# Kernel tuning notes

Hardware: AMD Instinct MI355X
Metric: run time of the kernel (lower is better)

The kernel has to match this reference:

```python
import jax, jax.numpy as jnp
import numpy as np

EPS = 1e-5

def _bn(x, g, b, m, v):
    # inference-mode BatchNorm2d over NCHW
    inv = g / jnp.sqrt(v + EPS)
    return x * inv[None, :, None, None] + (b - m * inv)[None, :, None, None]

def _adder2d(x, w, stride, pad):
    # AdderNet 'convolution': out = -sum_{c,kh,kw} |patch - w|
    B, C, H, W = x.shape
    O, _, k, _ = w.shape
    xp = jnp.pad(x, ((0, 0), (0, 0), (pad, pad), (pad, pad)))
    Ho = (H + 2 * pad - k) // stride + 1
    Wo = (W + 2 * pad - k) // stride + 1
    # unfold: [B, C, k*k, Ho, Wo] with (C, kh, kw) ordering matching w.reshape
    cols = jnp.stack([xp[:, :, i:i + stride * Ho:stride, j:j + stride * Wo:stride]
                      for i in range(k) for j in range(k)], axis=2)
    cols = cols.reshape(B, C * k * k, Ho * Wo)            # [B, CKK, L]
    wf = w.reshape(O, C * k * k)                          # [O, CKK]
    out = -jnp.sum(jnp.abs(cols[:, None, :, :] - wf[None, :, :, None]), axis=2)  # [B,O,L]
    return out.reshape(B, O, Ho, Wo)

def setup_inputs() -> dict:
    key = jax.random.key(0)
    ks = jax.random.split(key, 16)
    C = 64
    return {
        "x": jax.random.normal(ks[0], (4, C, 32, 32), jnp.float32),
        "bn1_g": jax.random.uniform(ks[1], (C,), jnp.float32),
        "bn1_b": jax.random.normal(ks[2], (C,), jnp.float32),
        "bn1_m": jax.random.normal(ks[3], (C,), jnp.float32),
        "bn1_v": jax.random.uniform(ks[4], (C,), jnp.float32),
        "w1": jax.random.normal(ks[5], (C, C, 3, 3), jnp.float32),
        "bn2_g": jax.random.uniform(ks[6], (C,), jnp.float32),
        "bn2_b": jax.random.normal(ks[7], (C,), jnp.float32),
        "bn2_m": jax.random.normal(ks[8], (C,), jnp.float32),
        "bn2_v": jax.random.uniform(ks[9], (C,), jnp.float32),
        "w2": jax.random.normal(ks[10], (C, C, 3, 3), jnp.float32),
        "fc1_w": jax.random.normal(ks[11], (C // 16, C), jnp.float32) * 0.1,
        "fc1_b": jax.random.normal(ks[12], (C // 16,), jnp.float32) * 0.1,
        "fc2_w": jax.random.normal(ks[13], (C, C // 16), jnp.float32) * 0.1,
        "fc2_b": jax.random.normal(ks[14], (C,), jnp.float32) * 0.1,
    }

def reference(x, bn1_g, bn1_b, bn1_m, bn1_v, w1,
              bn2_g, bn2_b, bn2_m, bn2_v, w2,
              fc1_w, fc1_b, fc2_w, fc2_b):
    out = jax.nn.relu(_bn(x, bn1_g, bn1_b, bn1_m, bn1_v))
    shortcut = x  # stride==1 and in_planes==planes -> identity shortcut
    out = _adder2d(out, w1, 1, 1)
    out = _adder2d(jax.nn.relu(_bn(out, bn2_g, bn2_b, bn2_m, bn2_v)), w2, 1, 1)
    # SE gate: global avg pool -> fc1 -> relu -> fc2 -> sigmoid
    s = out.mean(axis=(2, 3))                              # [B, planes]
    h = jax.nn.relu(s @ fc1_w.T + fc1_b)
    g = jax.nn.sigmoid(h @ fc2_w.T + fc2_b)
    return out * g[:, :, None, None] + shortcut
```

## Files before the change

kernel.cpp:

```cpp
#include <hip/hip_runtime.h>
#include <math.h>

#define NELEM   262144
#define NPAIRW  18432
#define PIMG    1296
#define PPADN   165888
#define NPAIR   147968
#define EPS_BN  1e-5f
#define QSC     128.0f
#define QBIAS_F 16384.5f
#define QZ_W    0x40004000u
#define QINV    (1.0f / 128.0f)

__device__ __forceinline__ unsigned sad16(unsigned a, unsigned b, unsigned acc) {
    asm("v_sad_u16 %0, %1, %2, %0" : "+v"(acc) : "v"(a), "v"(b));
    return acc;
}

__device__ __forceinline__ unsigned qu(float v) {
    return (unsigned)(int)fmaf(v, QSC, QBIAS_F);
}

__global__ __launch_bounds__(256) void prep_kernel(
    const float* __restrict__ x,
    const float* __restrict__ g1, const float* __restrict__ b1,
    const float* __restrict__ m1, const float* __restrict__ v1,
    const float* __restrict__ w1,
    const float* __restrict__ g2, const float* __restrict__ b2,
    const float* __restrict__ m2, const float* __restrict__ v2,
    const float* __restrict__ w2,
    unsigned* __restrict__ qxp, unsigned* __restrict__ qout1p,
    unsigned* __restrict__ qw1p, unsigned* __restrict__ qw2p,
    float* __restrict__ bn2c, float* __restrict__ sbuf)
{
    int i = blockIdx.x * 256 + threadIdx.x;
    if (i < NPAIR) {
        int bp  = i / 1156;
        int rc  = i - bp * 1156;
        int r   = rc / 34;
        int col = rc - r * 34;
        bool interior = (r > 0 && r < 33 && col > 0 && col < 33);
        unsigned q = QZ_W;
        if (interior) {
            int b  = bp >> 5;
            int c0 = (bp & 31) * 2;
            float inv0 = g1[c0] * rsqrtf(v1[c0] + EPS_BN);
            float bet0 = b1[c0] - m1[c0] * inv0;
            float inv1 = g1[c0 + 1] * rsqrtf(v1[c0 + 1] + EPS_BN);
            float bet1 = b1[c0 + 1] - m1[c0 + 1] * inv1;
            int off = (b * 64 + c0) * 1024 + (r - 1) * 32 + (col - 1);
            float a0 = fmaxf(fmaf(x[off],        inv0, bet0), 0.f);
            float a1 = fmaxf(fmaf(x[off + 1024], inv1, bet1), 0.f);
            q = qu(a0) | (qu(a1) << 16);
        }
        int pidx = bp * PIMG + r * 36 + col;
        qxp[pidx] = q;
        if (!interior) qout1p[pidx] = QZ_W;
        return;
    }
    int k = i - NPAIR;
    if (k < NPAIRW) {
        int o   = k / 288;
        int rem = k - o * 288;
        int pr  = rem / 9;
        int kk  = rem - pr * 9;
        int woff = (o * 64 + pr * 2) * 9 + kk;
        qw1p[k] = qu(w1[woff]) | (qu(w1[woff + 9]) << 16);
        return;
    }
    int l = k - NPAIRW;
    if (l < NPAIRW) {
        int o   = l / 288;
        int rem = l - o * 288;
        int pr  = rem / 9;
        int kk  = rem - pr * 9;
        int woff = (o * 64 + pr * 2) * 9 + kk;
        qw2p[l] = qu(w2[woff]) | (qu(w2[woff + 9]) << 16);
        return;
    }
    int m = l - NPAIRW;
    if (m < 64) {
        float inv = g2[m] * rsqrtf(v2[m] + EPS_BN);
        bn2c[m]      = -inv * QINV;
        bn2c[m + 64] = b2[m] - m2[m] * inv;
        return;
    }
    int s = m - 64;
    if (s >= 0 && s < 256) sbuf[s] = 0.f;
}

template<int MODE>
__global__ __launch_bounds__(256, 4) void adder_kernel(
    const unsigned* __restrict__ qsrc, const unsigned* __restrict__ qwp,
    const float* __restrict__ bn2c,
    unsigned* __restrict__ qout, float* __restrict__ fout,
    float* __restrict__ sbuf)
{
    __shared__ unsigned wlds[2][32][12];
    __shared__ unsigned red[16][16][16];

    const int blk = blockIdx.x;
    const int sp  = blk & 7;
    const int og  = (blk >> 3) & 31;
    const int b   = blk >> 8;
    const int t   = threadIdx.x;
    const int pos = t & 15;
    const int cq  = t >> 4;
    const int y_i = pos >> 2;
    const int x0  = (pos & 3) * 8;

    const unsigned* base = qsrc + (size_t)(b * 32 + cq * 2) * PIMG
                                + (sp * 4 + y_i) * 36 + x0;

    unsigned p[2][3][12];
#pragma unroll
    for (int r = 0; r < 3; ++r) {
        uint4 a0 = *reinterpret_cast<const uint4*>(base + r * 36);
        uint4 a1 = *reinterpret_cast<const uint4*>(base + r * 36 + 4);
        uint4 a2 = *reinterpret_cast<const uint4*>(base + r * 36 + 8);
        p[0][r][0] = a0.x; p[0][r][1]  = a0.y; p[0][r][2]  = a0.z; p[0][r][3]  = a0.w;
        p[0][r][4] = a1.x; p[0][r][5]  = a1.y; p[0][r][6]  = a1.z; p[0][r][7]  = a1.w;
        p[0][r][8] = a2.x; p[0][r][9]  = a2.y; p[0][r][10] = a2.z; p[0][r][11] = a2.w;
    }

    for (int i = t; i < 576; i += 256) {
        int o_i = i / 288;
        int rem = i - o_i * 288;
        int pr  = rem / 9;
        int kk  = rem - pr * 9;
        wlds[o_i][pr][kk] = qwp[((og * 2 + o_i) * 32 + pr) * 9 + kk];
    }
    __syncthreads();

    unsigned acc[2][8];
#pragma unroll
    for (int oo = 0; oo < 2; ++oo)
#pragma unroll
        for (int xi = 0; xi < 8; ++xi) acc[oo][xi] = 0u;

#pragma unroll
    for (int j = 0; j < 2; ++j) {
        if (j == 0) {
            const unsigned* pn = base + PIMG;
#pragma unroll
            for (int r = 0; r < 3; ++r) {
                uint4 a0 = *reinterpret_cast<const uint4*>(pn + r * 36);
                uint4 a1 = *reinterpret_cast<const uint4*>(pn + r * 36 + 4);
                uint4 a2 = *reinterpret_cast<const uint4*>(pn + r * 36 + 8);
                p[1][r][0] = a0.x; p[1][r][1]  = a0.y; p[1][r][2]  = a0.z; p[1][r][3]  = a0.w;
                p[1][r][4] = a1.x; p[1][r][5]  = a1.y; p[1][r][6]  = a1.z; p[1][r][7]  = a1.w;
                p[1][r][8] = a2.x; p[1][r][9]  = a2.y; p[1][r][10] = a2.z; p[1][r][11] = a2.w;
            }
        }
        const int pr = cq * 2 + j;
#pragma unroll
        for (int oo = 0; oo < 2; ++oo) {
            uint4 wa = *reinterpret_cast<const uint4*>(&wlds[oo][pr][0]);
            uint4 wb = *reinterpret_cast<const uint4*>(&wlds[oo][pr][4]);
            unsigned w8 = wlds[oo][pr][8];
            unsigned wv[9] = {wa.x, wa.y, wa.z, wa.w,
                              wb.x, wb.y, wb.z, wb.w, w8};
#pragma unroll
            for (int kh = 0; kh < 3; ++kh)
#pragma unroll
                for (int kw = 0; kw < 3; ++kw) {
                    unsigned ww = wv[kh * 3 + kw];
#pragma unroll
                    for (int xi = 0; xi < 8; ++xi)
                        acc[oo][xi] = sad16(p[j][kh][xi + kw], ww, acc[oo][xi]);
                }
        }
    }

    {
        unsigned* dst = &red[cq][pos][0];
        *reinterpret_cast<uint4*>(dst + 0)  = make_uint4(acc[0][0], acc[0][1], acc[0][2], acc[0][3]);
        *reinterpret_cast<uint4*>(dst + 4)  = make_uint4(acc[0][4], acc[0][5], acc[0][6], acc[0][7]);
        *reinterpret_cast<uint4*>(dst + 8)  = make_uint4(acc[1][0], acc[1][1], acc[1][2], acc[1][3]);
        *reinterpret_cast<uint4*>(dst + 12) = make_uint4(acc[1][4], acc[1][5], acc[1][6], acc[1][7]);
    }
    __syncthreads();

    const int oo2 = t >> 7;
    const int s   = t & 127;
    const int yy2 = s >> 5;
    const int xx2 = s & 31;
    const int pp  = yy2 * 4 + (xx2 >> 3);
    const int z   = (oo2 << 3) | (xx2 & 7);
    unsigned total = 0;
#pragma unroll
    for (int q = 0; q < 16; ++q) total += red[q][pp][z];

    const int o    = og * 2 + oo2;
    const int gy   = sp * 4 + yy2;
    const float accf = (float)total;

    if (MODE == 0) {
        float a2 = fmaxf(fmaf(accf, bn2c[o], bn2c[o + 64]), 0.f);
        unsigned short qv = (unsigned short)(int)fmaf(a2, QSC, QBIAS_F);
        size_t widx = (size_t)(b * 32 + (o >> 1)) * PIMG + (gy + 1) * 36 + (xx2 + 1);
        reinterpret_cast<unsigned short*>(qout)[widx * 2 + (o & 1)] = qv;
    } else {
        float v = -accf * QINV;
        fout[((b * 64 + o) * 32 + gy) * 32 + xx2] = v;
        float sum = v;
#pragma unroll
        for (int off = 32; off > 0; off >>= 1)
            sum += __shfl_down(sum, off, 64);
        if ((t & 63) == 0) atomicAdd(&sbuf[b * 64 + o], sum);
    }
}

__global__ __launch_bounds__(256) void gate_kernel(
    const float* __restrict__ out2, const float* __restrict__ x,
    const float* __restrict__ sbuf,
    const float* __restrict__ fc1w, const float* __restrict__ fc1b,
    const float* __restrict__ fc2w, const float* __restrict__ fc2b,
    float* __restrict__ out)
{
    const int bo = blockIdx.x;
    const int b  = bo >> 6;
    const int o  = bo & 63;
    const int t  = threadIdx.x;

    __shared__ float ss[64];
    if (t < 64) ss[t] = sbuf[b * 64 + t] * (1.f / 1024.f);
    __syncthreads();

    float h[4];
#pragma unroll
    for (int j = 0; j < 4; ++j) {
        float a = fc1b[j];
#pragma unroll
        for (int c = 0; c < 64; ++c) a += ss[c] * fc1w[j * 64 + c];
        h[j] = fmaxf(a, 0.f);
    }
    float zz = fc2b[o];
#pragma unroll
    for (int j = 0; j < 4; ++j) zz += h[j] * fc2w[o * 4 + j];
    float g = 1.f / (1.f + __expf(-zz));

    const int base = bo * 1024 + t * 4;
    float4 v  = *reinterpret_cast<const float4*>(out2 + base);
    float4 xv = *reinterpret_cast<const float4*>(x + base);
    float4 r;
    r.x = v.x * g + xv.x;
    r.y = v.y * g + xv.y;
    r.z = v.z * g + xv.z;
    r.w = v.w * g + xv.w;
    *reinterpret_cast<float4*>(out + base) = r;
}

extern "C" void kernel_launch(void* const* d_in, const int* in_sizes, int n_in,
                              void* d_out, int out_size, void* d_ws, size_t ws_size,
                              hipStream_t stream)
{
    const float* x    = (const float*)d_in[0];
    const float* bn1g = (const float*)d_in[1];
    const float* bn1b = (const float*)d_in[2];
    const float* bn1m = (const float*)d_in[3];
    const float* bn1v = (const float*)d_in[4];
    const float* w1   = (const float*)d_in[5];
    const float* bn2g = (const float*)d_in[6];
    const float* bn2b = (const float*)d_in[7];
    const float* bn2m = (const float*)d_in[8];
    const float* bn2v = (const float*)d_in[9];
    const float* w2   = (const float*)d_in[10];
    const float* fc1w = (const float*)d_in[11];
    const float* fc1b = (const float*)d_in[12];
    const float* fc2w = (const float*)d_in[13];
    const float* fc2b = (const float*)d_in[14];

    unsigned* ws     = (unsigned*)d_ws;
    unsigned* qxp    = ws;
    unsigned* qout1p = ws + PPADN;
    float*    out2   = (float*)(ws + 2 * PPADN);
    unsigned* qw1p   = ws + 2 * PPADN + NELEM;
    unsigned* qw2p   = ws + 2 * PPADN + NELEM + NPAIRW;
    float*    bn2c   = (float*)(ws + 2 * PPADN + NELEM + 2 * NPAIRW);
    float*    sbuf   = (float*)(ws + 2 * PPADN + NELEM + 2 * NPAIRW + 128);

    prep_kernel<<<724, 256, 0, stream>>>(x, bn1g, bn1b, bn1m, bn1v, w1,
                                         bn2g, bn2b, bn2m, bn2v, w2,
                                         qxp, qout1p, qw1p, qw2p, bn2c, sbuf);
    adder_kernel<0><<<1024, 256, 0, stream>>>(qxp,    qw1p, bn2c, qout1p, nullptr, nullptr);
    adder_kernel<1><<<1024, 256, 0, stream>>>(qout1p, qw2p, nullptr, nullptr, out2, sbuf);
    gate_kernel<<<256, 256, 0, stream>>>(out2, x, sbuf, fc1w, fc1b, fc2w, fc2b,
                                         (float*)d_out);
}
```

Measured before the change: 109.6 us.

## Fuse prep into adder kernels, computing BN1 and quantization into an LDS tile

Removes the separate prep kernel. The first adder kernel now applies BN1, ReLU and quantization to x directly into a padded shared-memory tile, shared through a union with the reduction buffer. Each kernel quantizes its own weights on the fly, and the first also writes the halo border and zeroes the SE sum buffer. This drops one launch and the global round-trip of the quantized input, at the cost of redundant BN and weight quantization across blocks and a larger shared-memory footprint.

```diff
diff --git a/kernel.cpp b/kernel.cpp
--- a/kernel.cpp
+++ b/kernel.cpp
@@ -2,10 +2,8 @@
 #include <math.h>
 
 #define NELEM   262144
-#define NPAIRW  18432
 #define PIMG    1296
 #define PPADN   165888
-#define NPAIR   147968
 #define EPS_BN  1e-5f
 #define QSC     128.0f
 #define QBIAS_F 16384.5f
@@ -16,88 +14,25 @@
     asm("v_sad_u16 %0, %1, %2, %0" : "+v"(acc) : "v"(a), "v"(b));
     return acc;
 }
-
 __device__ __forceinline__ unsigned qu(float v) {
     return (unsigned)(int)fmaf(v, QSC, QBIAS_F);
 }
 
-__global__ __launch_bounds__(256) void prep_kernel(
+__global__ __launch_bounds__(256, 4) void adder1_kernel(
     const float* __restrict__ x,
     const float* __restrict__ g1, const float* __restrict__ b1,
     const float* __restrict__ m1, const float* __restrict__ v1,
     const float* __restrict__ w1,
     const float* __restrict__ g2, const float* __restrict__ b2,
     const float* __restrict__ m2, const float* __restrict__ v2,
-    const float* __restrict__ w2,
-    unsigned* __restrict__ qxp, unsigned* __restrict__ qout1p,
-    unsigned* __restrict__ qw1p, unsigned* __restrict__ qw2p,
-    float* __restrict__ bn2c, float* __restrict__ sbuf)
+    unsigned* __restrict__ qout, float* __restrict__ sbuf)
 {
-    int i = blockIdx.x * 256 + threadIdx.x;
-    if (i < NPAIR) {
-        int bp  = i / 1156;
-        int rc  = i - bp * 1156;
-        int r   = rc / 34;
-        int col = rc - r * 34;
-        bool interior = (r > 0 && r < 33 && col > 0 && col < 33);
-        unsigned q = QZ_W;
-        if (interior) {
-            int b  = bp >> 5;
-            int c0 = (bp & 31) * 2;
-            float inv0 = g1[c0] * rsqrtf(v1[c0] + EPS_BN);
-            float bet0 = b1[c0] - m1[c0] * inv0;
-            float inv1 = g1[c0 + 1] * rsqrtf(v1[c0 + 1] + EPS_BN);
-            float bet1 = b1[c0 + 1] - m1[c0 + 1] * inv1;
-            int off = (b * 64 + c0) * 1024 + (r - 1) * 32 + (col - 1);
-            float a0 = fmaxf(fmaf(x[off],        inv0, bet0), 0.f);
-            float a1 = fmaxf(fmaf(x[off + 1024], inv1, bet1), 0.f);
-            q = qu(a0) | (qu(a1) << 16);
-        }
-        int pidx = bp * PIMG + r * 36 + col;
-        qxp[pidx] = q;
-        if (!interior) qout1p[pidx] = QZ_W;
-        return;
-    }
-    int k = i - NPAIR;
-    if (k < NPAIRW) {
-        int o   = k / 288;
-        int rem = k - o * 288;
-        int pr  = rem / 9;
-        int kk  = rem - pr * 9;
-        int woff = (o * 64 + pr * 2) * 9 + kk;
-        qw1p[k] = qu(w1[woff]) | (qu(w1[woff + 9]) << 16);
-        return;
-    }
-    int l = k - NPAIRW;
-    if (l < NPAIRW) {
-        int o   = l / 288;
-        int rem = l - o * 288;
-        int pr  = rem / 9;
-        int kk  = rem - pr * 9;
-        int woff = (o * 64 + pr * 2) * 9 + kk;
-        qw2p[l] = qu(w2[woff]) | (qu(w2[woff + 9]) << 16);
-        return;
-    }
-    int m = l - NPAIRW;
-    if (m < 64) {
-        float inv = g2[m] * rsqrtf(v2[m] + EPS_BN);
-        bn2c[m]      = -inv * QINV;
-        bn2c[m + 64] = b2[m] - m2[m] * inv;
-        return;
-    }
-    int s = m - 64;
-    if (s >= 0 && s < 256) sbuf[s] = 0.f;
-}
-
-template<int MODE>
-__global__ __launch_bounds__(256, 4) void adder_kernel(
-    const unsigned* __restrict__ qsrc, const unsigned* __restrict__ qwp,
-    const float* __restrict__ bn2c,
-    unsigned* __restrict__ qout, float* __restrict__ fout,
-    float* __restrict__ sbuf)
-{
+    __shared__ union {
+        unsigned tile[32][6][36];
+        unsigned red[16][16][16];
+    } sh;
     __shared__ unsigned wlds[2][32][12];
-    __shared__ unsigned red[16][16][16];
+    __shared__ float binv[64], bbeta[64];
 
     const int blk = blockIdx.x;
     const int sp  = blk & 7;
@@ -109,6 +44,149 @@
     const int y_i = pos >> 2;
     const int x0  = (pos & 3) * 8;
 
+    if (t < 64) {
+        float inv = g1[t] * rsqrtf(v1[t] + EPS_BN);
+        binv[t]  = inv;
+        bbeta[t] = b1[t] - m1[t] * inv;
+    }
+    for (int i = t; i < 576; i += 256) {
+        int o_i = i / 288;
+        int rem = i - o_i * 288;
+        int pr  = rem / 9;
+        int kk  = rem - pr * 9;
+        int woff = ((og * 2 + o_i) * 64 + pr * 2) * 9 + kk;
+        wlds[o_i][pr][kk] = qu(w1[woff]) | (qu(w1[woff + 9]) << 16);
+    }
+    if (og == 0) {
+        for (int i = sp * 256 + t; i < 32 * 132; i += 2048) {
+            int pair = i / 132;
+            int rem  = i - pair * 132;
+            int row, col;
+            if (rem < 34)       { row = 0;            col = rem;       }
+            else if (rem < 68)  { row = 33;           col = rem - 34;  }
+            else if (rem < 100) { row = rem - 68 + 1; col = 0;         }
+            else                { row = rem - 100 + 1; col = 33;       }
+            qout[(size_t)(b * 32 + pair) * PIMG + row * 36 + col] = QZ_W;
+        }
+    }
+    if (blk == 0) sbuf[t] = 0.f;
+    __syncthreads();
+
+    for (int i = t; i < 192; i += 256) {
+        int pair = i / 6;
+        int row  = i - pair * 6;
+        int gy   = sp * 4 - 1 + row;
+        unsigned* dst = &sh.tile[pair][row][0];
+        if (gy < 0 || gy > 31) {
+            for (int col = 0; col < 34; ++col) dst[col] = QZ_W;
+        } else {
+            dst[0] = QZ_W; dst[33] = QZ_W;
+            const int c0 = pair * 2;
+            const float inv0 = binv[c0],     bet0 = bbeta[c0];
+            const float inv1 = binv[c0 + 1], bet1 = bbeta[c0 + 1];
+            const float* px = x + (size_t)((b * 64 + c0) * 32 + gy) * 32;
+#pragma unroll
+            for (int gx = 0; gx < 32; gx += 4) {
+                float4 u0 = *reinterpret_cast<const float4*>(px + gx);
+                float4 u1 = *reinterpret_cast<const float4*>(px + 1024 + gx);
+                dst[1 + gx]     = qu(fmaxf(fmaf(u0.x, inv0, bet0), 0.f))
+                                | (qu(fmaxf(fmaf(u1.x, inv1, bet1), 0.f)) << 16);
+                dst[1 + gx + 1] = qu(fmaxf(fmaf(u0.y, inv0, bet0), 0.f))
+                                | (qu(fmaxf(fmaf(u1.y, inv1, bet1), 0.f)) << 16);
+                dst[1 + gx + 2] = qu(fmaxf(fmaf(u0.z, inv0, bet0), 0.f))
+                                | (qu(fmaxf(fmaf(u1.z, inv1, bet1), 0.f)) << 16);
+                dst[1 + gx + 3] = qu(fmaxf(fmaf(u0.w, inv0, bet0), 0.f))
+                                | (qu(fmaxf(fmaf(u1.w, inv1, bet1), 0.f)) << 16);
+            }
+        }
+    }
+    __syncthreads();
+
+    unsigned acc[2][8];
+#pragma unroll
+    for (int oo = 0; oo < 2; ++oo)
+#pragma unroll
+        for (int xi = 0; xi < 8; ++xi) acc[oo][xi] = 0u;
+
+#pragma unroll
+    for (int j = 0; j < 2; ++j) {
+        const int pr = cq * 2 + j;
+        unsigned p[3][12];
+#pragma unroll
+        for (int r = 0; r < 3; ++r) {
+            uint4 a0 = *reinterpret_cast<const uint4*>(&sh.tile[pr][y_i + r][x0]);
+            uint4 a1 = *reinterpret_cast<const uint4*>(&sh.tile[pr][y_i + r][x0 + 4]);
+            uint4 a2 = *reinterpret_cast<const uint4*>(&sh.tile[pr][y_i + r][x0 + 8]);
+            p[r][0] = a0.x; p[r][1]  = a0.y; p[r][2]  = a0.z; p[r][3]  = a0.w;
+            p[r][4] = a1.x; p[r][5]  = a1.y; p[r][6]  = a1.z; p[r][7]  = a1.w;
+            p[r][8] = a2.x; p[r][9]  = a2.y; p[r][10] = a2.z; p[r][11] = a2.w;
+        }
+#pragma unroll
+        for (int oo = 0; oo < 2; ++oo) {
+            uint4 wa = *reinterpret_cast<const uint4*>(&wlds[oo][pr][0]);
+            uint4 wb = *reinterpret_cast<const uint4*>(&wlds[oo][pr][4]);
+            unsigned w8 = wlds[oo][pr][8];
+            unsigned wv[9] = {wa.x, wa.y, wa.z, wa.w,
+                              wb.x, wb.y, wb.z, wb.w, w8};
+#pragma unroll
+            for (int kh = 0; kh < 3; ++kh)
+#pragma unroll
+                for (int kw = 0; kw < 3; ++kw) {
+                    unsigned ww = wv[kh * 3 + kw];
+#pragma unroll
+                    for (int xi = 0; xi < 8; ++xi)
+                        acc[oo][xi] = sad16(p[kh][xi + kw], ww, acc[oo][xi]);
+                }
+        }
+    }
+
+    __syncthreads();
+    {
+        unsigned* dst = &sh.red[cq][pos][0];
+        *reinterpret_cast<uint4*>(dst + 0)  = make_uint4(acc[0][0], acc[0][1], acc[0][2], acc[0][3]);
+        *reinterpret_cast<uint4*>(dst + 4)  = make_uint4(acc[0][4], acc[0][5], acc[0][6], acc[0][7]);
+        *reinterpret_cast<uint4*>(dst + 8)  = make_uint4(acc[1][0], acc[1][1], acc[1][2], acc[1][3]);
+        *reinterpret_cast<uint4*>(dst + 12) = make_uint4(acc[1][4], acc[1][5], acc[1][6], acc[1][7]);
+    }
+    __syncthreads();
+
+    const int oo2 = t >> 7;
+    const int s   = t & 127;
+    const int yy2 = s >> 5;
+    const int xx2 = s & 31;
+    const int pp  = yy2 * 4 + (xx2 >> 3);
+    const int z   = (oo2 << 3) | (xx2 & 7);
+    unsigned total = 0;
+#pragma unroll
+    for (int q = 0; q < 16; ++q) total += sh.red[q][pp][z];
+
+    const int o  = og * 2 + oo2;
+    const int gy = sp * 4 + yy2;
+    float inv2 = g2[o] * rsqrtf(v2[o] + EPS_BN);
+    float bet2 = b2[o] - m2[o] * inv2;
+    float a2 = fmaxf(fmaf((float)total, -inv2 * QINV, bet2), 0.f);
+    unsigned short qv = (unsigned short)(int)fmaf(a2, QSC, QBIAS_F);
+    size_t widx = (size_t)(b * 32 + (o >> 1)) * PIMG + (gy + 1) * 36 + (xx2 + 1);
+    reinterpret_cast<unsigned short*>(qout)[widx * 2 + (o & 1)] = qv;
+}
+
+__global__ __launch_bounds__(256, 4) void adder2_kernel(
+    const unsigned* __restrict__ qsrc, const float* __restrict__ w2,
+    float* __restrict__ fout, float* __restrict__ sbuf)
+{
+    __shared__ unsigned wlds[2][32][12];
+    __shared__ unsigned red[16][16][16];
+
+    const int blk = blockIdx.x;
+    const int sp  = blk & 7;
+    const int og  = (blk >> 3) & 31;
+    const int b   = blk >> 8;
+    const int t   = threadIdx.x;
+    const int pos = t & 15;
+    const int cq  = t >> 4;
+    const int y_i = pos >> 2;
+    const int x0  = (pos & 3) * 8;
+
     const unsigned* base = qsrc + (size_t)(b * 32 + cq * 2) * PIMG
                                 + (sp * 4 + y_i) * 36 + x0;
 
@@ -128,7 +206,8 @@
         int rem = i - o_i * 288;
         int pr  = rem / 9;
         int kk  = rem - pr * 9;
-        wlds[o_i][pr][kk] = qwp[((og * 2 + o_i) * 32 + pr) * 9 + kk];
+        int woff = ((og * 2 + o_i) * 64 + pr * 2) * 9 + kk;
+        wlds[o_i][pr][kk] = qu(w2[woff]) | (qu(w2[woff + 9]) << 16);
     }
     __syncthreads();
 
@@ -191,24 +270,15 @@
 #pragma unroll
     for (int q = 0; q < 16; ++q) total += red[q][pp][z];
 
-    const int o    = og * 2 + oo2;
-    const int gy   = sp * 4 + yy2;
-    const float accf = (float)total;
-
-    if (MODE == 0) {
-        float a2 = fmaxf(fmaf(accf, bn2c[o], bn2c[o + 64]), 0.f);
-        unsigned short qv = (unsigned short)(int)fmaf(a2, QSC, QBIAS_F);
-        size_t widx = (size_t)(b * 32 + (o >> 1)) * PIMG + (gy + 1) * 36 + (xx2 + 1);
-        reinterpret_cast<unsigned short*>(qout)[widx * 2 + (o & 1)] = qv;
-    } else {
-        float v = -accf * QINV;
-        fout[((b * 64 + o) * 32 + gy) * 32 + xx2] = v;
-        float sum = v;
-#pragma unroll
-        for (int off = 32; off > 0; off >>= 1)
-            sum += __shfl_down(sum, off, 64);
-        if ((t & 63) == 0) atomicAdd(&sbuf[b * 64 + o], sum);
-    }
+    const int o  = og * 2 + oo2;
+    const int gy = sp * 4 + yy2;
+    float v = -(float)total * QINV;
+    fout[((b * 64 + o) * 32 + gy) * 32 + xx2] = v;
+    float sum = v;
+#pragma unroll
+    for (int off = 32; off > 0; off >>= 1)
+        sum += __shfl_down(sum, off, 64);
+    if ((t & 63) == 0) atomicAdd(&sbuf[b * 64 + o], sum);
 }
 
 __global__ __launch_bounds__(256) void gate_kernel(
@@ -272,19 +342,14 @@
     const float* fc2b = (const float*)d_in[14];
 
     unsigned* ws     = (unsigned*)d_ws;
-    unsigned* qxp    = ws;
-    unsigned* qout1p = ws + PPADN;
-    float*    out2   = (float*)(ws + 2 * PPADN);
-    unsigned* qw1p   = ws + 2 * PPADN + NELEM;
-    unsigned* qw2p   = ws + 2 * PPADN + NELEM + NPAIRW;
-    float*    bn2c   = (float*)(ws + 2 * PPADN + NELEM + 2 * NPAIRW);
-    float*    sbuf   = (float*)(ws + 2 * PPADN + NELEM + 2 * NPAIRW + 128);
-
-    prep_kernel<<<724, 256, 0, stream>>>(x, bn1g, bn1b, bn1m, bn1v, w1,
-                                         bn2g, bn2b, bn2m, bn2v, w2,
-                                         qxp, qout1p, qw1p, qw2p, bn2c, sbuf);
-    adder_kernel<0><<<1024, 256, 0, stream>>>(qxp,    qw1p, bn2c, qout1p, nullptr, nullptr);
-    adder_kernel<1><<<1024, 256, 0, stream>>>(qout1p, qw2p, nullptr, nullptr, out2, sbuf);
+    unsigned* qout1p = ws;
+    float*    out2   = (float*)(ws + PPADN);
+    float*    sbuf   = (float*)(ws + PPADN + NELEM);
+
+    adder1_kernel<<<1024, 256, 0, stream>>>(x, bn1g, bn1b, bn1m, bn1v, w1,
+                                            bn2g, bn2b, bn2m, bn2v,
+                                            qout1p, sbuf);
+    adder2_kernel<<<1024, 256, 0, stream>>>(qout1p, w2, out2, sbuf);
     gate_kernel<<<256, 256, 0, stream>>>(out2, x, sbuf, fc1w, fc1b, fc2w, fc2b,
                                          (float*)d_out);
 }
```

Measured after the change: 117.3 us. 1.07x slower.

## Halve per-block spatial tile in adder kernel to double grid and occupancy

Applied to the files above, without the earlier changes.

Each adder block now covers 2 output rows instead of 4, and each thread computes 4 x-positions instead of 8. The grid doubles to 2048 blocks and launch bounds ask for 8 blocks per SM. Input patches are now loaded per channel-pair iteration instead of preloading both, which cuts register pressure. The trade-offs are more redundant halo loads and weight LDS fills per output, and only half the threads do the final reduction and store.

```diff
diff --git a/kernel.cpp b/kernel.cpp
--- a/kernel.cpp
+++ b/kernel.cpp
@@ -16,7 +16,6 @@
     asm("v_sad_u16 %0, %1, %2, %0" : "+v"(acc) : "v"(a), "v"(b));
     return acc;
 }
-
 __device__ __forceinline__ unsigned qu(float v) {
     return (unsigned)(int)fmaf(v, QSC, QBIAS_F);
 }
@@ -90,38 +89,27 @@
 }
 
 template<int MODE>
-__global__ __launch_bounds__(256, 4) void adder_kernel(
+__global__ __launch_bounds__(256, 8) void adder_kernel(
     const unsigned* __restrict__ qsrc, const unsigned* __restrict__ qwp,
     const float* __restrict__ bn2c,
     unsigned* __restrict__ qout, float* __restrict__ fout,
     float* __restrict__ sbuf)
 {
     __shared__ unsigned wlds[2][32][12];
-    __shared__ unsigned red[16][16][16];
+    __shared__ unsigned red[16][16][8];
 
     const int blk = blockIdx.x;
-    const int sp  = blk & 7;
-    const int og  = (blk >> 3) & 31;
-    const int b   = blk >> 8;
+    const int sp  = blk & 15;
+    const int og  = (blk >> 4) & 31;
+    const int b   = blk >> 9;
     const int t   = threadIdx.x;
     const int pos = t & 15;
     const int cq  = t >> 4;
-    const int y_i = pos >> 2;
-    const int x0  = (pos & 3) * 8;
+    const int y_i = pos >> 3;
+    const int x0  = (pos & 7) * 4;
 
     const unsigned* base = qsrc + (size_t)(b * 32 + cq * 2) * PIMG
-                                + (sp * 4 + y_i) * 36 + x0;
-
-    unsigned p[2][3][12];
-#pragma unroll
-    for (int r = 0; r < 3; ++r) {
-        uint4 a0 = *reinterpret_cast<const uint4*>(base + r * 36);
-        uint4 a1 = *reinterpret_cast<const uint4*>(base + r * 36 + 4);
-        uint4 a2 = *reinterpret_cast<const uint4*>(base + r * 36 + 8);
-        p[0][r][0] = a0.x; p[0][r][1]  = a0.y; p[0][r][2]  = a0.z; p[0][r][3]  = a0.w;
-        p[0][r][4] = a1.x; p[0][r][5]  = a1.y; p[0][r][6]  = a1.z; p[0][r][7]  = a1.w;
-        p[0][r][8] = a2.x; p[0][r][9]  = a2.y; p[0][r][10] = a2.z; p[0][r][11] = a2.w;
-    }
+                                + (sp * 2 + y_i) * 36 + x0;
 
     for (int i = t; i < 576; i += 256) {
         int o_i = i / 288;
@@ -132,25 +120,22 @@
     }
     __syncthreads();
 
-    unsigned acc[2][8];
+    unsigned acc[2][4];
 #pragma unroll
     for (int oo = 0; oo < 2; ++oo)
 #pragma unroll
-        for (int xi = 0; xi < 8; ++xi) acc[oo][xi] = 0u;
+        for (int xi = 0; xi < 4; ++xi) acc[oo][xi] = 0u;
 
 #pragma unroll
     for (int j = 0; j < 2; ++j) {
-        if (j == 0) {
-            const unsigned* pn = base + PIMG;
-#pragma unroll
-            for (int r = 0; r < 3; ++r) {
-                uint4 a0 = *reinterpret_cast<const uint4*>(pn + r * 36);
-                uint4 a1 = *reinterpret_cast<const uint4*>(pn + r * 36 + 4);
-                uint4 a2 = *reinterpret_cast<const uint4*>(pn + r * 36 + 8);
-                p[1][r][0] = a0.x; p[1][r][1]  = a0.y; p[1][r][2]  = a0.z; p[1][r][3]  = a0.w;
-                p[1][r][4] = a1.x; p[1][r][5]  = a1.y; p[1][r][6]  = a1.z; p[1][r][7]  = a1.w;
-                p[1][r][8] = a2.x; p[1][r][9]  = a2.y; p[1][r][10] = a2.z; p[1][r][11] = a2.w;
-            }
+        const unsigned* pc = base + j * PIMG;
+        unsigned p[3][6];
+#pragma unroll
+        for (int r = 0; r < 3; ++r) {
+            uint4 a0 = *reinterpret_cast<const uint4*>(pc + r * 36);
+            uint2 a1 = *reinterpret_cast<const uint2*>(pc + r * 36 + 4);
+            p[r][0] = a0.x; p[r][1] = a0.y; p[r][2] = a0.z; p[r][3] = a0.w;
+            p[r][4] = a1.x; p[r][5] = a1.y;
         }
         const int pr = cq * 2 + j;
 #pragma unroll
@@ -166,48 +151,46 @@
                 for (int kw = 0; kw < 3; ++kw) {
                     unsigned ww = wv[kh * 3 + kw];
 #pragma unroll
-                    for (int xi = 0; xi < 8; ++xi)
-                        acc[oo][xi] = sad16(p[j][kh][xi + kw], ww, acc[oo][xi]);
+                    for (int xi = 0; xi < 4; ++xi)
+                        acc[oo][xi] = sad16(p[kh][xi + kw], ww, acc[oo][xi]);
                 }
         }
     }
 
     {
         unsigned* dst = &red[cq][pos][0];
-        *reinterpret_cast<uint4*>(dst + 0)  = make_uint4(acc[0][0], acc[0][1], acc[0][2], acc[0][3]);
-        *reinterpret_cast<uint4*>(dst + 4)  = make_uint4(acc[0][4], acc[0][5], acc[0][6], acc[0][7]);
-        *reinterpret_cast<uint4*>(dst + 8)  = make_uint4(acc[1][0], acc[1][1], acc[1][2], acc[1][3]);
-        *reinterpret_cast<uint4*>(dst + 12) = make_uint4(acc[1][4], acc[1][5], acc[1][6], acc[1][7]);
+        *reinterpret_cast<uint4*>(dst)     = make_uint4(acc[0][0], acc[0][1], acc[0][2], acc[0][3]);
+        *reinterpret_cast<uint4*>(dst + 4) = make_uint4(acc[1][0], acc[1][1], acc[1][2], acc[1][3]);
     }
     __syncthreads();
 
-    const int oo2 = t >> 7;
-    const int s   = t & 127;
-    const int yy2 = s >> 5;
-    const int xx2 = s & 31;
-    const int pp  = yy2 * 4 + (xx2 >> 3);
-    const int z   = (oo2 << 3) | (xx2 & 7);
-    unsigned total = 0;
-#pragma unroll
-    for (int q = 0; q < 16; ++q) total += red[q][pp][z];
-
-    const int o    = og * 2 + oo2;
-    const int gy   = sp * 4 + yy2;
-    const float accf = (float)total;
-
-    if (MODE == 0) {
-        float a2 = fmaxf(fmaf(accf, bn2c[o], bn2c[o + 64]), 0.f);
-        unsigned short qv = (unsigned short)(int)fmaf(a2, QSC, QBIAS_F);
-        size_t widx = (size_t)(b * 32 + (o >> 1)) * PIMG + (gy + 1) * 36 + (xx2 + 1);
-        reinterpret_cast<unsigned short*>(qout)[widx * 2 + (o & 1)] = qv;
-    } else {
-        float v = -accf * QINV;
-        fout[((b * 64 + o) * 32 + gy) * 32 + xx2] = v;
-        float sum = v;
-#pragma unroll
-        for (int off = 32; off > 0; off >>= 1)
-            sum += __shfl_down(sum, off, 64);
-        if ((t & 63) == 0) atomicAdd(&sbuf[b * 64 + o], sum);
+    if (t < 128) {
+        const int oo2 = t >> 6;
+        const int yy2 = (t >> 5) & 1;
+        const int xx2 = t & 31;
+        const int pp  = yy2 * 8 + (xx2 >> 2);
+        const int z   = oo2 * 4 + (xx2 & 3);
+        unsigned total = 0;
+#pragma unroll
+        for (int q = 0; q < 16; ++q) total += red[q][pp][z];
+
+        const int o  = og * 2 + oo2;
+        const int gy = sp * 2 + yy2;
+
+        if (MODE == 0) {
+            float a2 = fmaxf(fmaf((float)total, bn2c[o], bn2c[o + 64]), 0.f);
+            unsigned short qv = (unsigned short)(int)fmaf(a2, QSC, QBIAS_F);
+            size_t widx = (size_t)(b * 32 + (o >> 1)) * PIMG + (gy + 1) * 36 + (xx2 + 1);
+            reinterpret_cast<unsigned short*>(qout)[widx * 2 + (o & 1)] = qv;
+        } else {
+            float v = -(float)total * QINV;
+            fout[((b * 64 + o) * 32 + gy) * 32 + xx2] = v;
+            float sum = v;
+#pragma unroll
+            for (int off = 32; off > 0; off >>= 1)
+                sum += __shfl_down(sum, off, 64);
+            if ((t & 63) == 0) atomicAdd(&sbuf[b * 64 + o], sum);
+        }
     }
 }
 
@@ -283,8 +266,8 @@
     prep_kernel<<<724, 256, 0, stream>>>(x, bn1g, bn1b, bn1m, bn1v, w1,
                                          bn2g, bn2b, bn2m, bn2v, w2,
                                          qxp, qout1p, qw1p, qw2p, bn2c, sbuf);
-    adder_kernel<0><<<1024, 256, 0, stream>>>(qxp,    qw1p, bn2c, qout1p, nullptr, nullptr);
-    adder_kernel<1><<<1024, 256, 0, stream>>>(qout1p, qw2p, nullptr, nullptr, out2, sbuf);
+    adder_kernel<0><<<2048, 256, 0, stream>>>(qxp,    qw1p, bn2c, qout1p, nullptr, nullptr);
+    adder_kernel<1><<<2048, 256, 0, stream>>>(qout1p, qw2p, nullptr, nullptr, out2, sbuf);
     gate_kernel<<<256, 256, 0, stream>>>(out2, x, sbuf, fc1w, fc1b, fc2w, fc2b,
                                          (float*)d_out);
 }
```

Measured after the change: 109.2 us. No clear change (-0.3%).
